# Performance work log

Hardware: AMD Instinct MI355X
Metric: run time of the kernel (lower is better)

The kernel has to match this reference:

```python
import jax, jax.numpy as jnp
import numpy as np

N, M, F_IN, F_OUT, B = 8192, 4096, 256, 128, 2048
NEG = -9e15
EPS = 1e-5


def leaky(x, slope=0.2):
    return jnp.where(x > 0, x, slope * x)


def batchnorm(x, gamma, beta):
    # BatchNorm1d training-mode semantics: biased batch stats over dim 0
    m = x.mean(axis=0)
    v = jnp.var(x, axis=0)
    return (x - m) * jax.lax.rsqrt(v + EPS) * gamma + beta


def setup_inputs() -> dict:
    key = jax.random.key(0)
    ks = jax.random.split(key, 12)
    inp = {}
    inp["Sinput"] = jax.random.normal(ks[0], (N, F_IN), dtype=jnp.float32)
    inp["Rinput"] = jax.random.normal(ks[1], (M, F_IN), dtype=jnp.float32)
    inp["inter_adj"] = jax.random.randint(ks[2], (N, M), 0, 2).astype(jnp.int32)
    inp["city_adj"] = jax.random.randint(ks[3], (N, N), 0, 2).astype(jnp.int32)
    inp["province_adj"] = jax.random.randint(ks[4], (N, N), 0, 2).astype(jnp.int32)
    inp["source_index"] = jax.random.randint(ks[5], (B,), 0, N).astype(jnp.int32)
    s_w = 1.414 * np.sqrt(6.0 / (F_IN + F_OUT))  # xavier_uniform gain=1.414
    s_a = 1.414 * np.sqrt(6.0 / (2 * F_OUT + 1))
    inp["W1"] = jax.random.uniform(ks[6], (F_IN, F_OUT), jnp.float32, -s_w, s_w)
    inp["W2"] = jax.random.uniform(ks[7], (F_IN, F_OUT), jnp.float32, -s_w, s_w)
    inp["a"] = jax.random.uniform(ks[8], (2 * F_OUT, 1), jnp.float32, -s_a, s_a)
    inp["a3"] = jax.random.uniform(ks[9], (2 * F_OUT, 1), jnp.float32, -s_a, s_a)
    inp["a4"] = jax.random.uniform(ks[10], (2 * F_OUT, 1), jnp.float32, -s_a, s_a)
    inp["bn1_gamma"] = jnp.ones((F_OUT,), jnp.float32)
    inp["bn1_beta"] = jnp.zeros((F_OUT,), jnp.float32)
    inp["bn2_gamma"] = jnp.ones((F_OUT,), jnp.float32)
    inp["bn2_beta"] = jnp.zeros((F_OUT,), jnp.float32)
    return inp


def reference(Sinput, Rinput, inter_adj, city_adj, province_adj, source_index,
              W1, W2, a, a3, a4, bn1_gamma, bn1_beta, bn2_gamma, bn2_beta):
    F = W1.shape[1]
    h1 = Rinput @ W1            # [M, F]
    h2 = Sinput @ W2            # [N, F]
    # Decomposed GAT score: cat([h1[m], h2[n]]) @ a == h1[m]@a[:F] + h2[n]@a[F:]
    e12 = leaky((h2 @ a[F:, 0])[:, None] + (h1 @ a[:F, 0])[None, :])  # [N, M]
    att_inter = jax.nn.softmax(jnp.where(inter_adj > 0, e12, NEG), axis=1)
    h2_ = h2[source_index]      # [B, F]
    # cat([h2_, h2_]) @ a3 -> h2_ @ (a3[:F] + a3[F:]), constant along N axis
    s3 = leaky(h2_ @ (a3[:F, 0] + a3[F:, 0]))  # [B]
    s4 = leaky(h2_ @ (a4[:F, 0] + a4[F:, 0]))  # [B]
    Nn = Sinput.shape[0]
    e3 = jnp.broadcast_to(s3[:, None], (s3.shape[0], Nn))
    e4 = jnp.broadcast_to(s4[:, None], (s4.shape[0], Nn))
    att3 = jax.nn.softmax(jnp.where(city_adj[source_index] > 0, e3, NEG), axis=1)
    att4 = jax.nn.softmax(jnp.where(province_adj[source_index] > 0, e4, NEG), axis=1)
    InterRC = att_inter @ h1                    # [N, F]
    IntraNC = att3.T @ h2_ + att4.T @ h2_       # [N, F]
    v_output = leaky(batchnorm(att_inter.T @ h2, bn1_gamma, bn1_beta))  # [M, F]
    u_output = leaky(batchnorm(InterRC + IntraNC, bn2_gamma, bn2_beta))  # [N, F]
    h_prime = u_output @ v_output.T             # [N, M]
    return jax.nn.elu(h_prime)
```

## Files before the change

kernel.cpp:

```cpp
#include <hip/hip_runtime.h>
#include <stdint.h>

#define N_ 8192
#define M_ 4096
#define FIN_ 256
#define F_ 128
#define B_ 2048

typedef __attribute__((ext_vector_type(8))) short vs8;
typedef __attribute__((ext_vector_type(8))) __bf16 vb8;
typedef __attribute__((ext_vector_type(4))) float vf4;

union ABu { vs8 s; vb8 b; };

__device__ __forceinline__ vf4 mfma16(const ABu& a, const ABu& b, vf4 c) {
    return __builtin_amdgcn_mfma_f32_16x16x32_bf16(a.b, b.b, c, 0, 0, 0);
}
__device__ __forceinline__ unsigned short f2b(float x) {
    union { float f; unsigned u; } v; v.f = x;
    unsigned r = v.u + 0x7fffu + ((v.u >> 16) & 1u);
    return (unsigned short)(r >> 16);
}
__device__ __forceinline__ float lrelu(float x) { return x > 0.f ? x : 0.2f * x; }

__global__ void k_prep(const float* __restrict__ W1, const float* __restrict__ W2,
                       unsigned short* __restrict__ W1T, unsigned short* __restrict__ W2T,
                       float4* __restrict__ Z, int nz4) {
    int id = blockIdx.x * 256 + threadIdx.x;
    if (id < 65536) {
        const float* W = (id < 32768) ? W1 : W2;
        unsigned short* WT = (id < 32768) ? W1T : W2T;
        int o = id & 32767;
        int f = o >> 8, k = o & 255;
        WT[o] = f2b(W[k * F_ + f]);
    } else {
        int z = id - 65536;
        if (z < nz4) Z[z] = make_float4(0.f, 0.f, 0.f, 0.f);
    }
}

__global__ __launch_bounds__(256) void k_hgemmF(const float* __restrict__ Rin, const float* __restrict__ Sin,
                                                const unsigned short* __restrict__ W1T,
                                                const unsigned short* __restrict__ W2T,
                                                const float* __restrict__ a,
                                                float* __restrict__ h2,
                                                unsigned short* __restrict__ h1P, unsigned short* __restrict__ h2P,
                                                float* __restrict__ s1, float* __restrict__ s2) {
    __shared__ unsigned short tb[16][136];
    __shared__ float sred[4][16];
    int t = threadIdx.x;
    int w = t >> 6, l = t & 63, lr = l & 15, lg = l >> 4;
    int gr = blockIdx.x * 16;
    const float* X; const unsigned short* WT; unsigned short* HP; float* sout; const float* av;
    int row0; bool isH2;
    if (gr < M_) { X = Rin; WT = W1T; HP = h1P; sout = s1; av = a;      row0 = gr;      isH2 = false; }
    else         { X = Sin; WT = W2T; HP = h2P; sout = s2; av = a + F_; row0 = gr - M_; isH2 = true;  }
    int fbase = w * 32;
    vf4 acc[2] = {};
    const float* xp = X + (size_t)(row0 + lr) * FIN_ + lg * 8;
#pragma unroll
    for (int kk = 0; kk < FIN_; kk += 32) {
        float4 xa = *(const float4*)(xp + kk);
        float4 xb = *(const float4*)(xp + kk + 4);
        ABu af;
        af.s[0] = (short)f2b(xa.x); af.s[1] = (short)f2b(xa.y);
        af.s[2] = (short)f2b(xa.z); af.s[3] = (short)f2b(xa.w);
        af.s[4] = (short)f2b(xb.x); af.s[5] = (short)f2b(xb.y);
        af.s[6] = (short)f2b(xb.z); af.s[7] = (short)f2b(xb.w);
#pragma unroll
        for (int q = 0; q < 2; ++q) {
            ABu bf; bf.s = *(const vs8*)(WT + (fbase + q * 16 + lr) * FIN_ + kk + lg * 8);
            acc[q] = mfma16(af, bf, acc[q]);
        }
    }
    if (isH2) {
#pragma unroll
        for (int q = 0; q < 2; ++q)
#pragma unroll
            for (int r = 0; r < 4; ++r)
                h2[(size_t)(row0 + lg * 4 + r) * F_ + fbase + q * 16 + lr] = acc[q][r];
    }
#pragma unroll
    for (int q = 0; q < 2; ++q)
#pragma unroll
        for (int r = 0; r < 4; ++r)
            tb[lg * 4 + r][fbase + q * 16 + lr] = f2b(acc[q][r]);
    float a0 = av[fbase + lr], a1 = av[fbase + 16 + lr];
    float tv[4];
#pragma unroll
    for (int r = 0; r < 4; ++r) tv[r] = acc[0][r] * a0 + acc[1][r] * a1;
#pragma unroll
    for (int off = 1; off < 16; off <<= 1)
#pragma unroll
        for (int r = 0; r < 4; ++r) tv[r] += __shfl_xor(tv[r], off, 64);
    if ((l & 15) == 0)
#pragma unroll
        for (int r = 0; r < 4; ++r) sred[w][lg * 4 + r] = tv[r];
    __syncthreads();
    {
        int f = t >> 1, half = t & 1;
        vs8 o;
#pragma unroll
        for (int j = 0; j < 8; ++j) o[j] = (short)tb[half * 8 + j][f];
        *(vs8*)(HP + ((size_t)(row0 >> 5) * 128 + f) * 32 + (row0 & 16) + half * 8) = o;
    }
    if (t < 16) {
        float s = sred[0][t] + sred[1][t] + sred[2][t] + sred[3][t];
        sout[row0 + t] = s;
    }
}

__global__ __launch_bounds__(256) void k_adjgather(const int* __restrict__ inter, const float* __restrict__ s1,
                                                   const float* __restrict__ s2, unsigned short* __restrict__ bm,
                                                   float* __restrict__ rowmax, float* __restrict__ rowinv,
                                                   const int* __restrict__ city, const int* __restrict__ prov,
                                                   const int* __restrict__ src,
                                                   uint32_t* __restrict__ BMtc, uint32_t* __restrict__ BMtp,
                                                   float* __restrict__ w3, float* __restrict__ w4,
                                                   const float* __restrict__ h2, unsigned short* __restrict__ h2wP) {
    __shared__ float wred[8];
    int t = threadIdx.x;
    int wv = t >> 6, ln = t & 63;
    if (blockIdx.x < N_) {
        int n = blockIdx.x;
        const int* rp = inter + (size_t)n * M_ + t * 16;
        float sv[16]; unsigned mask = 0;
#pragma unroll
        for (int c = 0; c < 4; ++c) {
            int4 v = *(const int4*)(rp + c * 4);
            if (v.x > 0) mask |= 1u << (c * 4 + 0);
            if (v.y > 0) mask |= 1u << (c * 4 + 1);
            if (v.z > 0) mask |= 1u << (c * 4 + 2);
            if (v.w > 0) mask |= 1u << (c * 4 + 3);
            float4 s = *(const float4*)(s1 + t * 16 + c * 4);
            sv[c * 4 + 0] = s.x; sv[c * 4 + 1] = s.y; sv[c * 4 + 2] = s.z; sv[c * 4 + 3] = s.w;
        }
        bm[(size_t)n * 256 + t] = (unsigned short)(mask & 0xffffu);
        float mx = -3.0e38f;
#pragma unroll
        for (int j = 0; j < 16; ++j) if (mask & (1u << j)) mx = fmaxf(mx, sv[j]);
        for (int off = 32; off > 0; off >>= 1) mx = fmaxf(mx, __shfl_down(mx, off, 64));
        if (ln == 0) wred[wv] = mx;
        __syncthreads();
        float s1mx = fmaxf(fmaxf(wred[0], wred[1]), fmaxf(wred[2], wred[3]));
        float s2n = s2[n];
        float rmx = lrelu(s2n + s1mx);
        float sum = 0.f;
#pragma unroll
        for (int j = 0; j < 16; ++j) if (mask & (1u << j)) sum += __expf(lrelu(s2n + sv[j]) - rmx);
        for (int off = 32; off > 0; off >>= 1) sum += __shfl_down(sum, off, 64);
        if (ln == 0) wred[4 + wv] = sum;
        __syncthreads();
        if (t == 0) {
            float tot = wred[4] + wred[5] + wred[6] + wred[7];
            bool any = s1mx > -2.9e38f;
            rowmax[n] = any ? rmx : 0.f;
            rowinv[n] = (any && tot > 0.f) ? 1.0f / tot : 0.f;
        }
    } else if (blockIdx.x < N_ + 2 * B_) {
        int bb = blockIdx.x - N_;
        int b = bb & (B_ - 1);
        bool isC = bb < B_;
        const int* adj = isC ? city : prov;
        uint32_t* BM = isC ? BMtc : BMtp;
        float* wout = isC ? w3 : w4;
        const int* rowp = adj + (size_t)src[b] * N_;
        int cnt = 0;
#pragma unroll 4
        for (int i = 0; i < N_ / 256; ++i) {
            int v = rowp[i * 256 + t];
            unsigned long long bal = __ballot(v > 0);
            cnt += (v > 0);
            if (ln == 0) {
                int widx = i * 8 + wv * 2;
                BM[(size_t)widx * B_ + b] = (uint32_t)bal;
                BM[(size_t)(widx + 1) * B_ + b] = (uint32_t)(bal >> 32);
            }
        }
        float fc = (float)cnt;
        for (int off = 32; off > 0; off >>= 1) fc += __shfl_down(fc, off, 64);
        if (ln == 0) wred[wv] = fc;
        __syncthreads();
        if (t == 0) {
            float tot = wred[0] + wred[1] + wred[2] + wred[3];
            wout[b] = tot > 0.f ? 1.0f / tot : 0.f;
        }
    } else {
        int bblk = blockIdx.x - (N_ + 2 * B_);
        int f = t & 127, halfb = t >> 7;
        vs8 o0, o1;
#pragma unroll
        for (int i = 0; i < 8; ++i) {
            int b0 = bblk * 32 + halfb * 16 + i;
            o0[i] = (short)f2b(h2[(size_t)src[b0] * F_ + f]);
            int b1 = b0 + 8;
            o1[i] = (short)f2b(h2[(size_t)src[b1] * F_ + f]);
        }
        unsigned short* dst = h2wP + ((size_t)bblk * 128 + f) * 32 + halfb * 16;
        *(vs8*)dst = o0;
        *(vs8*)(dst + 8) = o1;
    }
}

__global__ __launch_bounds__(256) void k_attmat2(const unsigned char* __restrict__ bm8,
                                                 const float* __restrict__ s1, const float* __restrict__ s2,
                                                 const float* __restrict__ rowmax, const float* __restrict__ rowinv,
                                                 unsigned short* __restrict__ attP,
                                                 unsigned short* __restrict__ attT) {
    __shared__ unsigned short tile[64][33];
    int bx = blockIdx.x;
    int mt = bx & 63, nt = bx >> 6;
    int nb = nt * 32, mb = mt * 64;
    int t = threadIdx.x;
    int mo = t & 7, nl = t >> 3;
    int n = nb + nl;
    int m = mb + mo * 8;
    unsigned bits = bm8[(size_t)n * 512 + (m >> 3)];
    float s2n = s2[n], rmx = rowmax[n], rin = rowinv[n];
    float4 sa = *(const float4*)(s1 + m);
    float4 sb = *(const float4*)(s1 + m + 4);
    float sv[8] = {sa.x, sa.y, sa.z, sa.w, sb.x, sb.y, sb.z, sb.w};
    vs8 o;
#pragma unroll
    for (int j = 0; j < 8; ++j) {
        float v = (bits & (1u << j)) ? __expf(lrelu(s2n + sv[j]) - rmx) * rin : 0.f;
        o[j] = (short)f2b(v);
        tile[mo * 8 + j][nl] = (unsigned short)o[j];
    }
    *(vs8*)(attP + ((size_t)(m >> 5) * N_ + n) * 32 + (m & 31)) = o;
    __syncthreads();
    int mr = t >> 2, sg = t & 3;
    vs8 ot;
#pragma unroll
    for (int j = 0; j < 8; ++j) ot[j] = (short)tile[mr][sg * 8 + j];
    *(vs8*)(attT + ((size_t)nt * M_ + mb + mr) * 32 + sg * 8) = ot;
}

__global__ __launch_bounds__(256) void k_gemmABC(const unsigned short* __restrict__ attP,
                                                 const unsigned short* __restrict__ attT,
                                                 const unsigned short* __restrict__ h1P,
                                                 const unsigned short* __restrict__ h2P,
                                                 const uint32_t* __restrict__ BMtc, const uint32_t* __restrict__ BMtp,
                                                 const float* __restrict__ w3, const float* __restrict__ w4,
                                                 const unsigned short* __restrict__ h2wP,
                                                 float* __restrict__ uP, float* __restrict__ vP) {
    int t = threadIdx.x;
    int w = t >> 6, l = t & 63;
    int lr = l & 15, lg = l >> 4;
    int bx = blockIdx.x;
    if (bx < 1024) {
        bool isA = bx < 512;
        int i = isA ? bx : bx - 512;
        int x, y, kbase;
        const unsigned short* Asrc; const unsigned short* Bsrc; float* Out;
        if (isA) { x = i & 127; y = i >> 7; kbase = y * 32;
                   Asrc = attP; Bsrc = h1P; Out = uP + (size_t)y * N_ * F_; }
        else     { x = i & 63;  y = i >> 6; kbase = y * 32;
                   Asrc = attT; Bsrc = h2P; Out = vP + (size_t)y * M_ * F_; }
        int rb0 = x * 64 + (w & 1) * 32;
        int fb = (w >> 1) * 64;
        vf4 acc[2][4] = {};
        int rowsK = isA ? N_ : M_;
        size_t aoff = (size_t)(rb0 + lr) * 32 + lg * 8;
        const unsigned short* apm = Asrc + (size_t)kbase * rowsK * 32 + aoff;
        size_t astride = (size_t)rowsK * 32;
        ABu a0, a1;
        a0.s = *(const vs8*)apm;
        a1.s = *(const vs8*)(apm + 16 * 32);
        for (int it = 0; it < 32; ++it) {
            const unsigned short* hb = Bsrc + (size_t)(kbase + it) * 128 * 32;
            ABu b0, b1, b2, b3;
            b0.s = *(const vs8*)(hb + (size_t)(fb + lr) * 32 + lg * 8);
            b1.s = *(const vs8*)(hb + (size_t)(fb + 16 + lr) * 32 + lg * 8);
            b2.s = *(const vs8*)(hb + (size_t)(fb + 32 + lr) * 32 + lg * 8);
            b3.s = *(const vs8*)(hb + (size_t)(fb + 48 + lr) * 32 + lg * 8);
            const unsigned short* apn = apm + (it < 31 ? astride : 0);
            ABu a0n, a1n;
            a0n.s = *(const vs8*)apn;
            a1n.s = *(const vs8*)(apn + 16 * 32);
            acc[0][0] = mfma16(a0, b0, acc[0][0]);
            acc[1][0] = mfma16(a1, b0, acc[1][0]);
            acc[0][1] = mfma16(a0, b1, acc[0][1]);
            acc[1][1] = mfma16(a1, b1, acc[1][1]);
            acc[0][2] = mfma16(a0, b2, acc[0][2]);
            acc[1][2] = mfma16(a1, b2, acc[1][2]);
            acc[0][3] = mfma16(a0, b3, acc[0][3]);
            acc[1][3] = mfma16(a1, b3, acc[1][3]);
            a0 = a0n; a1 = a1n;
            apm = apn;
        }
#pragma unroll
        for (int s = 0; s < 2; ++s)
#pragma unroll
            for (int q = 0; q < 4; ++q)
#pragma unroll
                for (int r = 0; r < 4; ++r)
                    Out[(size_t)(rb0 + s * 16 + lg * 4 + r) * F_ + fb + q * 16 + lr] = acc[s][q][r];
    } else {
        int i = bx - 1024;
        int xc = i & 127, yc = i >> 7;
        int nb0 = xc * 64 + (w & 1) * 32;
        int fb = (w >> 1) * 64;
        int wi = nb0 >> 5;
        const uint32_t* bc = BMtc + (size_t)wi * B_;
        const uint32_t* bp = BMtp + (size_t)wi * B_;
        vf4 acc[2][4] = {};
        int b0s = yc * (B_ / 4);
        for (int b0 = b0s; b0 < b0s + B_ / 4; b0 += 32) {
            int bb = b0 + lg * 8;
            uint4 c0 = *(const uint4*)(bc + bb);
            uint4 c1 = *(const uint4*)(bc + bb + 4);
            uint4 p0 = *(const uint4*)(bp + bb);
            uint4 p1 = *(const uint4*)(bp + bb + 4);
            float4 wa = *(const float4*)(w3 + bb);
            float4 wb = *(const float4*)(w3 + bb + 4);
            float4 wc = *(const float4*)(w4 + bb);
            float4 wd = *(const float4*)(w4 + bb + 4);
            const unsigned short* hb = h2wP + (size_t)(b0 >> 5) * 128 * 32;
            ABu bf0, bf1, bf2, bf3;
            bf0.s = *(const vs8*)(hb + (size_t)(fb + lr) * 32 + lg * 8);
            bf1.s = *(const vs8*)(hb + (size_t)(fb + 16 + lr) * 32 + lg * 8);
            bf2.s = *(const vs8*)(hb + (size_t)(fb + 32 + lr) * 32 + lg * 8);
            bf3.s = *(const vs8*)(hb + (size_t)(fb + 48 + lr) * 32 + lg * 8);
            uint32_t cw[8] = {c0.x, c0.y, c0.z, c0.w, c1.x, c1.y, c1.z, c1.w};
            uint32_t pw[8] = {p0.x, p0.y, p0.z, p0.w, p1.x, p1.y, p1.z, p1.w};
            float w3v[8] = {wa.x, wa.y, wa.z, wa.w, wb.x, wb.y, wb.z, wb.w};
            float w4v[8] = {wc.x, wc.y, wc.z, wc.w, wd.x, wd.y, wd.z, wd.w};
            ABu af0, af1;
#pragma unroll
            for (int j = 0; j < 8; ++j) {
                float v0 = (((cw[j] >> lr) & 1u) ? w3v[j] : 0.f) + (((pw[j] >> lr) & 1u) ? w4v[j] : 0.f);
                float v1 = (((cw[j] >> (16 + lr)) & 1u) ? w3v[j] : 0.f) + (((pw[j] >> (16 + lr)) & 1u) ? w4v[j] : 0.f);
                af0.s[j] = (short)f2b(v0);
                af1.s[j] = (short)f2b(v1);
            }
            acc[0][0] = mfma16(af0, bf0, acc[0][0]);
            acc[1][0] = mfma16(af1, bf0, acc[1][0]);
            acc[0][1] = mfma16(af0, bf1, acc[0][1]);
            acc[1][1] = mfma16(af1, bf1, acc[1][1]);
            acc[0][2] = mfma16(af0, bf2, acc[0][2]);
            acc[1][2] = mfma16(af1, bf2, acc[1][2]);
            acc[0][3] = mfma16(af0, bf3, acc[0][3]);
            acc[1][3] = mfma16(af1, bf3, acc[1][3]);
        }
        float* Out = uP + (size_t)(4 + yc) * N_ * F_;
#pragma unroll
        for (int s = 0; s < 2; ++s)
#pragma unroll
            for (int q = 0; q < 4; ++q)
#pragma unroll
                for (int r = 0; r < 4; ++r)
                    Out[(size_t)(nb0 + s * 16 + lg * 4 + r) * F_ + fb + q * 16 + lr] = acc[s][q][r];
    }
}

__global__ __launch_bounds__(256) void k_bnreduce(const float* __restrict__ vP, const float* __restrict__ uP,
                                                  float* __restrict__ v_in, float* __restrict__ u_in,
                                                  float* __restrict__ stats) {
    __shared__ float r1[256], r2[256];
    int bx = blockIdx.x;
    const float* P; float* O; int R, nb_; size_t stride; float* sum; float* sq;
    if (bx < 256) { P = vP; O = v_in; R = M_; nb_ = 256; stride = (size_t)M_ * F_;
                    sum = stats; sq = stats + 128; }
    else          { P = uP; O = u_in; R = N_; nb_ = 512; stride = (size_t)N_ * F_;
                    sum = stats + 256; sq = stats + 384; bx -= 256; }
    int f = threadIdx.x & 127;
    int half = threadIdx.x >> 7;
    float s = 0.f, s2v = 0.f;
    for (int r = bx * 2 + half; r < R; r += nb_ * 2) {
        float v = 0.f;
#pragma unroll
        for (int y = 0; y < 8; ++y) v += P[(size_t)y * stride + (size_t)r * F_ + f];
        O[(size_t)r * F_ + f] = v;
        s += v; s2v += v * v;
    }
    r1[threadIdx.x] = s; r2[threadIdx.x] = s2v;
    __syncthreads();
    if (half == 0) {
        atomicAdd(&sum[f], r1[f] + r1[f + 128]);
        atomicAdd(&sq[f], r2[f] + r2[f + 128]);
    }
}

__global__ __launch_bounds__(256) void k_bnapplyF(const float* __restrict__ v_in, const float* __restrict__ u_in,
                                                  const float* __restrict__ stats,
                                                  const float* __restrict__ g1, const float* __restrict__ b1,
                                                  const float* __restrict__ g2, const float* __restrict__ b2,
                                                  unsigned short* __restrict__ v_outb, unsigned short* __restrict__ u_outb) {
    __shared__ float sc[256], sh[256];
    int t = threadIdx.x;
    {
        int which = t >> 7, f = t & 127;
        const float* sum = stats + which * 256;
        const float* sq = sum + 128;
        const float* g = which ? g2 : g1;
        const float* be = which ? b2 : b1;
        float R = which ? (float)N_ : (float)M_;
        float mean = sum[f] / R;
        float var = sq[f] / R - mean * mean;
        float s = g[f] * rsqrtf(var + 1e-5f);
        sc[t] = s; sh[t] = be[f] - mean * s;
    }
    __syncthreads();
    int id4 = blockIdx.x * 256 + t;
    int idx = id4 * 4;
    int which = idx >= M_ * F_;
    int rel = which ? idx - M_ * F_ : idx;
    const float* P = which ? u_in : v_in;
    unsigned short* Q = which ? u_outb : v_outb;
    int f0 = (rel & 127) + which * 128;
    float4 p = *(const float4*)(P + rel);
    ushort4 o;
    o.x = f2b(lrelu(p.x * sc[f0 + 0] + sh[f0 + 0]));
    o.y = f2b(lrelu(p.y * sc[f0 + 1] + sh[f0 + 1]));
    o.z = f2b(lrelu(p.z * sc[f0 + 2] + sh[f0 + 2]));
    o.w = f2b(lrelu(p.w * sc[f0 + 3] + sh[f0 + 3]));
    *(ushort4*)(Q + rel) = o;
}

__global__ __launch_bounds__(256) void k_gemmD(const unsigned short* __restrict__ U,
                                               const unsigned short* __restrict__ V,
                                               float* __restrict__ out) {
    int w = threadIdx.x >> 6, l = threadIdx.x & 63;
    int lr = l & 15, lg = l >> 4;
    int nb = blockIdx.x * 64 + w * 16;
    int mb = blockIdx.y * 64;
    vf4 acc[4] = {};
#pragma unroll
    for (int k0 = 0; k0 < F_; k0 += 32) {
        ABu af; af.s = *(const vs8*)(U + (size_t)(nb + lr) * F_ + k0 + lg * 8);
#pragma unroll
        for (int q = 0; q < 4; ++q) {
            ABu bf; bf.s = *(const vs8*)(V + (size_t)(mb + q * 16 + lr) * F_ + k0 + lg * 8);
            acc[q] = mfma16(af, bf, acc[q]);
        }
    }
#pragma unroll
    for (int q = 0; q < 4; ++q)
#pragma unroll
        for (int r = 0; r < 4; ++r) {
            int row = nb + lg * 4 + r;
            int col = mb + q * 16 + lr;
            float x = acc[q][r];
            out[(size_t)row * M_ + col] = x > 0.f ? x : __expf(x) - 1.f;
        }
}

extern "C" void kernel_launch(void* const* d_in, const int* in_sizes, int n_in,
                              void* d_out, int out_size, void* d_ws, size_t ws_size,
                              hipStream_t stream) {
    const float* Sinput = (const float*)d_in[0];
    const float* Rinput = (const float*)d_in[1];
    const int* inter_adj = (const int*)d_in[2];
    const int* city_adj = (const int*)d_in[3];
    const int* prov_adj = (const int*)d_in[4];
    const int* src = (const int*)d_in[5];
    const float* W1 = (const float*)d_in[6];
    const float* W2 = (const float*)d_in[7];
    const float* a = (const float*)d_in[8];
    const float* g1 = (const float*)d_in[11];
    const float* b1 = (const float*)d_in[12];
    const float* g2 = (const float*)d_in[13];
    const float* b2 = (const float*)d_in[14];
    float* out = (float*)d_out;

    char* ws = (char*)d_ws;
    size_t o = 0;
    auto take = [&](size_t bytes) { char* p = ws + o; o += (bytes + 255) & ~(size_t)255; return p; };
    float* stats = (float*)take(512 * 4);
    size_t zero_bytes = o;
    float* u_in = (float*)take((size_t)N_ * F_ * 4);
    float* v_in = (float*)take((size_t)M_ * F_ * 4);
    float* uP = (float*)take((size_t)8 * N_ * F_ * 4);
    float* vP = (float*)take((size_t)8 * M_ * F_ * 4);
    float* h2 = (float*)take((size_t)N_ * F_ * 4);
    unsigned short* h1P = (unsigned short*)take((size_t)(M_ / 32) * 128 * 32 * 2);
    unsigned short* h2P = (unsigned short*)take((size_t)(N_ / 32) * 128 * 32 * 2);
    unsigned short* W1T = (unsigned short*)take((size_t)F_ * FIN_ * 2);
    unsigned short* W2T = (unsigned short*)take((size_t)F_ * FIN_ * 2);
    float* s1 = (float*)take(M_ * 4);
    float* s2 = (float*)take(N_ * 4);
    float* rowmax = (float*)take(N_ * 4);
    float* rowinv = (float*)take(N_ * 4);
    float* w3 = (float*)take(B_ * 4);
    float* w4 = (float*)take(B_ * 4);
    unsigned short* h2wP = (unsigned short*)take((size_t)(B_ / 32) * 128 * 32 * 2);
    unsigned short* u_outb = (unsigned short*)take((size_t)N_ * F_ * 2);
    unsigned short* v_outb = (unsigned short*)take((size_t)M_ * F_ * 2);
    uint32_t* BMtc = (uint32_t*)take((size_t)256 * B_ * 4);
    uint32_t* BMtp = (uint32_t*)take((size_t)256 * B_ * 4);
    unsigned short* bm = (unsigned short*)take((size_t)N_ * 256 * 2);
    unsigned short* attP = (unsigned short*)take((size_t)N_ * M_ * 2);
    unsigned short* attT = (unsigned short*)take((size_t)N_ * M_ * 2);
    (void)ws_size; (void)in_sizes; (void)n_in; (void)out_size;

    int nz4 = (int)(zero_bytes / 16);
    int zblocks = (nz4 + 255) / 256;
    k_prep<<<256 + zblocks, 256, 0, stream>>>(W1, W2, W1T, W2T, (float4*)d_ws, nz4);
    k_hgemmF<<<(M_ + N_) / 16, 256, 0, stream>>>(Rinput, Sinput, W1T, W2T, a, h2, h1P, h2P, s1, s2);
    k_adjgather<<<N_ + 2 * B_ + B_ / 32, 256, 0, stream>>>(inter_adj, s1, s2, bm, rowmax, rowinv,
                                                           city_adj, prov_adj, src, BMtc, BMtp, w3, w4,
                                                           h2, h2wP);
    k_attmat2<<<16384, 256, 0, stream>>>((const unsigned char*)bm, s1, s2, rowmax, rowinv, attP, attT);
    k_gemmABC<<<1536, 256, 0, stream>>>(attP, attT, h1P, h2P, BMtc, BMtp, w3, w4, h2wP, uP, vP);
    k_bnreduce<<<768, 256, 0, stream>>>(vP, uP, v_in, u_in, stats);
    k_bnapplyF<<<(M_ + N_) * F_ / 4 / 256, 256, 0, stream>>>(v_in, u_in, stats, g1, b1, g2, b2, v_outb, u_outb);
    k_gemmD<<<dim3(N_ / 64, M_ / 64), 256, 0, stream>>>(u_outb, v_outb, out);
}
```

Measured before the change: 347.8 us.

## Stage GEMM A/B tiles through double-buffered LDS via global_load_lds

The attention-by-feature GEMM branch now copies A and B tiles into a double-buffered shared-memory area with direct global-to-LDS loads, two k-blocks per step. The next step's copy overlaps the MFMAs on the current buffer. This replaces per-wave redundant global loads of B (and A), so waves in a block share data instead of each fetching it. It costs 48KB of LDS per block, which may lower occupancy, and adds two barriers per step. LDS reads may also hit bank conflicts because of the 64-byte row stride.

```diff
diff --git a/kernel.cpp b/kernel.cpp
--- a/kernel.cpp
+++ b/kernel.cpp
@@ -22,6 +22,11 @@
     return (unsigned short)(r >> 16);
 }
 __device__ __forceinline__ float lrelu(float x) { return x > 0.f ? x : 0.2f * x; }
+
+__device__ __forceinline__ void glds16(const unsigned short* g, void* l) {
+    __builtin_amdgcn_global_load_lds((const __attribute__((address_space(1))) unsigned int*)g,
+                                     (__attribute__((address_space(3))) unsigned int*)l, 16, 0, 0);
+}
 
 __global__ void k_prep(const float* __restrict__ W1, const float* __restrict__ W2,
                        unsigned short* __restrict__ W1T, unsigned short* __restrict__ W2T,
@@ -244,6 +249,7 @@
                                                  const float* __restrict__ w3, const float* __restrict__ w4,
                                                  const unsigned short* __restrict__ h2wP,
                                                  float* __restrict__ uP, float* __restrict__ vP) {
+    __shared__ __align__(16) unsigned short smem[24576];
     int t = threadIdx.x;
     int w = t >> 6, l = t & 63;
     int lr = l & 15, lg = l >> 4;
@@ -251,43 +257,63 @@
     if (bx < 1024) {
         bool isA = bx < 512;
         int i = isA ? bx : bx - 512;
-        int x, y, kbase;
+        int x, y, rowsK;
         const unsigned short* Asrc; const unsigned short* Bsrc; float* Out;
-        if (isA) { x = i & 127; y = i >> 7; kbase = y * 32;
-                   Asrc = attP; Bsrc = h1P; Out = uP + (size_t)y * N_ * F_; }
-        else     { x = i & 63;  y = i >> 6; kbase = y * 32;
-                   Asrc = attT; Bsrc = h2P; Out = vP + (size_t)y * M_ * F_; }
-        int rb0 = x * 64 + (w & 1) * 32;
+        if (isA) { x = i & 127; y = i >> 7; Asrc = attP; Bsrc = h1P;
+                   Out = uP + (size_t)y * N_ * F_; rowsK = N_; }
+        else     { x = i & 63;  y = i >> 6; Asrc = attT; Bsrc = h2P;
+                   Out = vP + (size_t)y * M_ * F_; rowsK = M_; }
+        int kbase = y * 32;
+        int rb0b = x * 64;
+        int rh = (w & 1) * 32;
         int fb = (w >> 1) * 64;
+        int ch0 = w * 6;
+        auto stage = [&](int step, int curb) {
+#pragma unroll
+            for (int ii = 0; ii < 6; ++ii) {
+                int c = ch0 + ii;
+                const unsigned short* g; int loff;
+                if (c < 8) {
+                    int kb = c >> 2;
+                    g = Asrc + (size_t)(kbase + 2 * step + kb) * rowsK * 32 + rb0b * 32
+                        + (c & 3) * 512 + l * 8;
+                    loff = curb * 24576 + kb * 4096 + (c & 3) * 1024;
+                } else {
+                    int c2 = c - 8;
+                    int kb = c2 >> 3;
+                    g = Bsrc + (size_t)(kbase + 2 * step + kb) * 4096 + (c2 & 7) * 512 + l * 8;
+                    loff = curb * 24576 + 8192 + kb * 8192 + (c2 & 7) * 1024;
+                }
+                glds16(g, (char*)smem + loff);
+            }
+        };
         vf4 acc[2][4] = {};
-        int rowsK = isA ? N_ : M_;
-        size_t aoff = (size_t)(rb0 + lr) * 32 + lg * 8;
-        const unsigned short* apm = Asrc + (size_t)kbase * rowsK * 32 + aoff;
-        size_t astride = (size_t)rowsK * 32;
-        ABu a0, a1;
-        a0.s = *(const vs8*)apm;
-        a1.s = *(const vs8*)(apm + 16 * 32);
-        for (int it = 0; it < 32; ++it) {
-            const unsigned short* hb = Bsrc + (size_t)(kbase + it) * 128 * 32;
-            ABu b0, b1, b2, b3;
-            b0.s = *(const vs8*)(hb + (size_t)(fb + lr) * 32 + lg * 8);
-            b1.s = *(const vs8*)(hb + (size_t)(fb + 16 + lr) * 32 + lg * 8);
-            b2.s = *(const vs8*)(hb + (size_t)(fb + 32 + lr) * 32 + lg * 8);
-            b3.s = *(const vs8*)(hb + (size_t)(fb + 48 + lr) * 32 + lg * 8);
-            const unsigned short* apn = apm + (it < 31 ? astride : 0);
-            ABu a0n, a1n;
-            a0n.s = *(const vs8*)apn;
-            a1n.s = *(const vs8*)(apn + 16 * 32);
-            acc[0][0] = mfma16(a0, b0, acc[0][0]);
-            acc[1][0] = mfma16(a1, b0, acc[1][0]);
-            acc[0][1] = mfma16(a0, b1, acc[0][1]);
-            acc[1][1] = mfma16(a1, b1, acc[1][1]);
-            acc[0][2] = mfma16(a0, b2, acc[0][2]);
-            acc[1][2] = mfma16(a1, b2, acc[1][2]);
-            acc[0][3] = mfma16(a0, b3, acc[0][3]);
-            acc[1][3] = mfma16(a1, b3, acc[1][3]);
-            a0 = a0n; a1 = a1n;
-            apm = apn;
+        stage(0, 0);
+        __syncthreads();
+        int cur = 0;
+        for (int step = 0; step < 16; ++step) {
+            if (step < 15) stage(step + 1, cur ^ 1);
+            const char* base = (const char*)smem + cur * 24576;
+#pragma unroll
+            for (int kb = 0; kb < 2; ++kb) {
+                ABu a0, a1, b0, b1, b2, b3;
+                a0.s = *(const vs8*)(base + kb * 4096 + (rh + lr) * 64 + lg * 16);
+                a1.s = *(const vs8*)(base + kb * 4096 + (rh + 16 + lr) * 64 + lg * 16);
+                b0.s = *(const vs8*)(base + 8192 + kb * 8192 + (fb + lr) * 64 + lg * 16);
+                b1.s = *(const vs8*)(base + 8192 + kb * 8192 + (fb + 16 + lr) * 64 + lg * 16);
+                b2.s = *(const vs8*)(base + 8192 + kb * 8192 + (fb + 32 + lr) * 64 + lg * 16);
+                b3.s = *(const vs8*)(base + 8192 + kb * 8192 + (fb + 48 + lr) * 64 + lg * 16);
+                acc[0][0] = mfma16(a0, b0, acc[0][0]);
+                acc[1][0] = mfma16(a1, b0, acc[1][0]);
+                acc[0][1] = mfma16(a0, b1, acc[0][1]);
+                acc[1][1] = mfma16(a1, b1, acc[1][1]);
+                acc[0][2] = mfma16(a0, b2, acc[0][2]);
+                acc[1][2] = mfma16(a1, b2, acc[1][2]);
+                acc[0][3] = mfma16(a0, b3, acc[0][3]);
+                acc[1][3] = mfma16(a1, b3, acc[1][3]);
+            }
+            __syncthreads();
+            cur ^= 1;
         }
 #pragma unroll
         for (int s = 0; s < 2; ++s)
@@ -295,7 +321,7 @@
             for (int q = 0; q < 4; ++q)
 #pragma unroll
                 for (int r = 0; r < 4; ++r)
-                    Out[(size_t)(rb0 + s * 16 + lg * 4 + r) * F_ + fb + q * 16 + lr] = acc[s][q][r];
+                    Out[(size_t)(rb0b + rh + s * 16 + lg * 4 + r) * F_ + fb + q * 16 + lr] = acc[s][q][r];
     } else {
         int i = bx - 1024;
         int xc = i & 127, yc = i >> 7;
```

Result: faster. 327.0 us (-6.0%).
